# Performance work log

Hardware: AMD Instinct MI355X
Metric: run time of the kernel (lower is better)

## Reference

```python
import jax, jax.numpy as jnp
import numpy as np

N, T, C, G, E = 50000, 2, 768, 16, 800000
H = C // 4          # 192
OUT = 3
EPS = 1e-5


def _lin_init(k, fan_in, fan_out):
    s = 1.0 / np.sqrt(fan_in)
    kw, kb = jax.random.split(k)
    W = jax.random.uniform(kw, (fan_in, fan_out), minval=-s, maxval=s, dtype=jnp.float32)
    b = jax.random.uniform(kb, (fan_out,), minval=-s, maxval=s, dtype=jnp.float32)
    return W, b


def setup_inputs() -> dict:
    key = jax.random.key(0)
    ks = jax.random.split(key, 8)
    x = jax.random.normal(ks[0], (N, T, C), dtype=jnp.float32)
    batch = jnp.sort(jax.random.randint(ks[1], (N,), 0, G))
    edge_index = jax.random.randint(ks[2], (2, E), 0, N)
    W0, b0 = _lin_init(ks[3], C, H)
    W1, b1 = _lin_init(ks[4], H, H)
    Wh1, bh1 = _lin_init(ks[5], H, H)
    Wh2, bh2 = _lin_init(ks[6], H, OUT)
    ones = jnp.ones((H,), jnp.float32)
    zeros = jnp.zeros((H,), jnp.float32)
    return {
        "x": x, "batch": batch, "edge_index": edge_index,
        "W0": W0, "b0": b0, "gn0_w": ones, "gn0_b": zeros, "gn0_a": ones,
        "W1": W1, "b1": b1, "gn1_w": ones, "gn1_b": zeros, "gn1_a": ones,
        "Wh1": Wh1, "bh1": bh1, "Wh2": Wh2, "bh2": bh2,
    }


def _gelu(v):
    return jax.nn.gelu(v, approximate=False)  # torch nn.GELU default = exact erf


def _gcn_conv(h, W, b, src, dst, dinv):
    # PyG GCNConv: x' = D^-1/2 (A+I) D^-1/2 (x W) + b, self-loops added implicitly
    h = jnp.einsum('ntc,cd->ntd', h, W)                       # [N,T,Cout]
    norm = (dinv[src] * dinv[dst])[:, None, None]             # [E,1,1]
    agg = jax.ops.segment_sum(h[src] * norm, dst, num_segments=N)
    agg = agg + h * (dinv * dinv)[:, None, None]              # self-loop term
    return agg + b


def _graph_norm(h, batch, cnt, w, b, alpha):
    # PyG GraphNorm: per-graph mean/var with learnable mean scale
    mean = jax.ops.segment_sum(h, batch, num_segments=G) / cnt   # [G,T,C]
    out = h - alpha * mean[batch]
    var = jax.ops.segment_sum(out * out, batch, num_segments=G) / cnt
    std = jnp.sqrt(var + EPS)
    return w * out / std[batch] + b


def reference(x, batch, edge_index,
              W0, b0, gn0_w, gn0_b, gn0_a,
              W1, b1, gn1_w, gn1_b, gn1_a,
              Wh1, bh1, Wh2, bh2):
    src, dst = edge_index[0], edge_index[1]
    deg = jax.ops.segment_sum(jnp.ones((E,), jnp.float32), dst, num_segments=N) + 1.0
    dinv = jax.lax.rsqrt(deg)
    cnt = jax.ops.segment_sum(jnp.ones((N,), jnp.float32), batch, num_segments=G)[:, None, None]

    # layer 0: 768 -> 192 (no residual, shape mismatch)
    h = _gcn_conv(x, W0, b0, src, dst, dinv)
    h = _gelu(_graph_norm(h, batch, cnt, gn0_w, gn0_b, gn0_a))
    # layer 1: 192 -> 192 with residual
    h_in = h
    h = _gcn_conv(h, W1, b1, src, dst, dinv)
    h = _gelu(_graph_norm(h, batch, cnt, gn1_w, gn1_b, gn1_a))
    h = h + h_in
    # MLP head
    h = _gelu(jnp.einsum('ntc,cd->ntd', h, Wh1) + bh1)
    out = jnp.einsum('ntc,cd->ntd', h, Wh2) + bh2            # [N,T,3]
    return out
```

## Files before the change

### kernel.cpp

```cpp
#include <hip/hip_runtime.h>
#include <math.h>

#define NN   50000
#define TT   2
#define CC   768
#define GG   16
#define EE   800000
#define HH   192
#define OUTD 3
#define MR   (NN*TT)
#define FD   (TT*HH)
#define EPS_GN 1e-5f
#define GN_CHUNK 128
#define AGG_CH 128

typedef __attribute__((ext_vector_type(8))) short bf16x8;
typedef __attribute__((ext_vector_type(4))) float f32x4;

__device__ __forceinline__ float gelu_exact(float x){
    return 0.5f * x * (1.0f + erff(x * 0.70710678118654752440f));
}

__device__ __forceinline__ short f2b(float f){
    unsigned u = __float_as_uint(f);
    unsigned r = (u + 0x7FFFu + ((u>>16)&1u)) >> 16;
    return (short)r;
}
__device__ __forceinline__ float b2f(unsigned short u){
    return __uint_as_float(((unsigned)u)<<16);
}

__global__ __launch_bounds__(256) void k_deg(const int* __restrict__ dst, float* __restrict__ deg){
    int e = blockIdx.x*256 + threadIdx.x;
    if(e < EE) atomicAdd(&deg[dst[e]], 1.0f);
}

__global__ __launch_bounds__(64) void k_cnt2(const int* __restrict__ batch, float* __restrict__ cnt){
    int g = threadIdx.x;
    if(g >= GG) return;
    int lo0=0, hi=NN;
    while(lo0<hi){ int mid=(lo0+hi)>>1; if(batch[mid] < g) lo0=mid+1; else hi=mid; }
    int lo1=lo0; hi=NN;
    while(lo1<hi){ int mid=(lo1+hi)>>1; if(batch[mid] < g+1) lo1=mid+1; else hi=mid; }
    cnt[g] = (float)(lo1 - lo0);
}

__global__ __launch_bounds__(256) void k_dinv(const float* __restrict__ deg, float* __restrict__ dinv){
    int i = blockIdx.x*256 + threadIdx.x;
    if(i < NN) dinv[i] = rsqrtf(deg[i] + 1.0f);
}

__global__ __launch_bounds__(256) void k_wconv(const float* __restrict__ W0, const float* __restrict__ W1,
                                               const float* __restrict__ Wh1,
                                               short* __restrict__ Wt0, short* __restrict__ Wt1,
                                               short* __restrict__ Wth1){
    int i = blockIdx.x*256 + threadIdx.x;
    if(i < CC*HH){
        int k = i / HH, n = i % HH;
        Wt0[(size_t)n*CC + k] = f2b(W0[i]);
    }
    if(i < HH*HH){
        int k = i / HH, n = i % HH;
        Wt1 [(size_t)n*HH + k] = f2b(W1[i]);
        Wth1[(size_t)n*HH + k] = f2b(Wh1[i]);
    }
}

__global__ __launch_bounds__(256) void k_scan1(const float* __restrict__ deg, int* __restrict__ partial){
    __shared__ int s[256];
    int t = threadIdx.x;
    int i = blockIdx.x*256 + t;
    int v = (i < NN) ? (int)deg[i] : 0;
    s[t] = v; __syncthreads();
    for(int off=128; off>0; off>>=1){ if(t < off) s[t] += s[t+off]; __syncthreads(); }
    if(t == 0) partial[blockIdx.x] = s[0];
}

__global__ __launch_bounds__(256) void k_scan2(int* __restrict__ partial){
    __shared__ int s[256];
    int t = threadIdx.x;
    int v = partial[t];
    s[t] = v; __syncthreads();
    for(int off=1; off<256; off<<=1){
        int x = (t >= off) ? s[t-off] : 0;
        __syncthreads();
        s[t] += x;
        __syncthreads();
    }
    partial[t] = s[t] - v;
}

__global__ __launch_bounds__(256) void k_scan3(const float* __restrict__ deg, const int* __restrict__ partial,
                                               int* __restrict__ csr_off){
    __shared__ int s[256];
    int t = threadIdx.x;
    int i = blockIdx.x*256 + t;
    int v = (i < NN) ? (int)deg[i] : 0;
    s[t] = v; __syncthreads();
    for(int off=1; off<256; off<<=1){
        int x = (t >= off) ? s[t-off] : 0;
        __syncthreads();
        s[t] += x;
        __syncthreads();
    }
    if(i < NN) csr_off[i] = partial[blockIdx.x] + s[t] - v;
}

__global__ __launch_bounds__(256) void k_fill(const int* __restrict__ src, const int* __restrict__ dst,
                                              const int* __restrict__ csr_off, int* __restrict__ fillcnt,
                                              int* __restrict__ csr_src){
    int e = blockIdx.x*256 + threadIdx.x;
    if(e < EE){
        int d = dst[e];
        int pos = csr_off[d] + atomicAdd(&fillcnt[d], 1);
        csr_src[pos] = src[e];
    }
}

__device__ __forceinline__ void gn8(const float* __restrict__ src,
                                    const float* __restrict__ sm, const float* __restrict__ sq,
                                    int sb, int hb_,
                                    const float* __restrict__ wg, const float* __restrict__ bg,
                                    const float* __restrict__ ag, float ic, float v[8]){
    float4 u0 = *(const float4*)(src),     u1 = *(const float4*)(src+4);
    float4 m0 = *(const float4*)(sm+sb),   m1 = *(const float4*)(sm+sb+4);
    float4 q0 = *(const float4*)(sq+sb),   q1 = *(const float4*)(sq+sb+4);
    float4 w0 = *(const float4*)(wg+hb_),  w1 = *(const float4*)(wg+hb_+4);
    float4 b0 = *(const float4*)(bg+hb_),  b1 = *(const float4*)(bg+hb_+4);
    float4 a0 = *(const float4*)(ag+hb_),  a1 = *(const float4*)(ag+hb_+4);
    float uu[8]={u0.x,u0.y,u0.z,u0.w,u1.x,u1.y,u1.z,u1.w};
    float mm[8]={m0.x,m0.y,m0.z,m0.w,m1.x,m1.y,m1.z,m1.w};
    float qq[8]={q0.x,q0.y,q0.z,q0.w,q1.x,q1.y,q1.z,q1.w};
    float ww[8]={w0.x,w0.y,w0.z,w0.w,w1.x,w1.y,w1.z,w1.w};
    float bb[8]={b0.x,b0.y,b0.z,b0.w,b1.x,b1.y,b1.z,b1.w};
    float aa[8]={a0.x,a0.y,a0.z,a0.w,a1.x,a1.y,a1.z,a1.w};
    #pragma unroll
    for(int j=0;j<8;j++){
        float mean = mm[j]*ic, ex2 = qq[j]*ic, al = aa[j];
        float var = ex2 - (2.0f*al - al*al)*mean*mean;
        float t = ww[j]*(uu[j] - al*mean)*rsqrtf(var + EPS_GN) + bb[j];
        v[j] = gelu_exact(t);
    }
}

template<int MODE, int NORM, bool BIAS>
__global__ __launch_bounds__(256) void k_gemm_mfma(
        const float* __restrict__ A1, const float* __restrict__ A0,
        const short* __restrict__ Bt,
        const float* __restrict__ bias, void* __restrict__ Cv,
        const float* __restrict__ W2, const float* __restrict__ b2,
        const int* __restrict__ batch, const float* __restrict__ cnt,
        const float* __restrict__ sm1, const float* __restrict__ sq1,
        const float* __restrict__ wg1, const float* __restrict__ bg1, const float* __restrict__ ag1,
        const float* __restrict__ sm0, const float* __restrict__ sq0,
        const float* __restrict__ wg0, const float* __restrict__ bg0, const float* __restrict__ ag0,
        int Mrows, int Kdim){
    __shared__ short As[64][40];
    __shared__ short Bs[192][40];
    int tid = threadIdx.x;
    int bm = blockIdx.x*64;
    int wv = tid>>6, lane = tid&63;
    int lm = lane&15, lq = lane>>4;

    f32x4 acc[12];
    #pragma unroll
    for(int i=0;i<12;i++) acc[i] = (f32x4){0.f,0.f,0.f,0.f};

    int ar = tid>>2, akg = (tid&3)<<3;
    int row = bm + ar;
    bool aok = row < Mrows;
    const float* Ap1 = A1 + (size_t)row*Kdim + akg;
    const float* Ap0 = (NORM==2) ? (A0 + (size_t)row*Kdim + akg) : nullptr;
    int g = 0, tT = 0; float ic = 0.f;
    if(NORM >= 1 && aok){
        int nn = row>>1; tT = row&1;
        g = batch[nn];
        ic = 1.0f / cnt[g];
    }

    for(int k0 = 0; k0 < Kdim; k0 += 32){
        bf16x8 ap = {};
        if(aok){
            if(NORM == 0){
                float4 av0 = *(const float4*)(Ap1 + k0);
                float4 av1 = *(const float4*)(Ap1 + k0 + 4);
                ap[0]=f2b(av0.x); ap[1]=f2b(av0.y); ap[2]=f2b(av0.z); ap[3]=f2b(av0.w);
                ap[4]=f2b(av1.x); ap[5]=f2b(av1.y); ap[6]=f2b(av1.z); ap[7]=f2b(av1.w);
            } else {
                int hb_ = akg + k0;
                int sb  = g*FD + tT*HH + hb_;
                float v[8];
                gn8(Ap1 + k0, sm1, sq1, sb, hb_, wg1, bg1, ag1, ic, v);
                if(NORM == 2){
                    float v0[8];
                    gn8(Ap0 + k0, sm0, sq0, sb, hb_, wg0, bg0, ag0, ic, v0);
                    #pragma unroll
                    for(int j=0;j<8;j++) v[j] += v0[j];
                }
                #pragma unroll
                for(int j=0;j<8;j++) ap[j] = f2b(v[j]);
            }
        }
        bf16x8 bvals[3];
        #pragma unroll
        for(int i=0;i<3;i++){
            int idx = tid + i*256;
            int n = idx>>2, kg = (idx&3)<<3;
            bvals[i] = *(const bf16x8*)(Bt + (size_t)n*Kdim + k0 + kg);
        }
        __syncthreads();
        *(bf16x8*)&As[ar][akg] = ap;
        #pragma unroll
        for(int i=0;i<3;i++){
            int idx = tid + i*256;
            int n = idx>>2, kg = (idx&3)<<3;
            *(bf16x8*)&Bs[n][kg] = bvals[i];
        }
        __syncthreads();
        bf16x8 af = *(const bf16x8*)&As[wv*16 + lm][lq*8];
        #pragma unroll
        for(int ct=0; ct<12; ct++){
            bf16x8 bfr = *(const bf16x8*)&Bs[ct*16 + lm][lq*8];
            acc[ct] = __builtin_amdgcn_mfma_f32_16x16x32_bf16(af, bfr, acc[ct], 0, 0, 0);
        }
    }

    if(MODE == 1){
        short* C = (short*)Cv;
        #pragma unroll
        for(int ct=0; ct<12; ct++){
            int col = ct*16 + lm;
            float bs = BIAS ? bias[col] : 0.f;
            #pragma unroll
            for(int r=0; r<4; r++){
                int orow = bm + wv*16 + lq*4 + r;
                if(orow < Mrows) C[(size_t)orow*HH + col] = f2b(acc[ct][r] + bs);
            }
        }
    } else {
        float hs[4][3] = {};
        #pragma unroll
        for(int ct=0; ct<12; ct++){
            int col = ct*16 + lm;
            float bs = bias[col];
            float w20 = W2[col*3+0], w21 = W2[col*3+1], w22 = W2[col*3+2];
            #pragma unroll
            for(int r=0; r<4; r++){
                float gl = gelu_exact(acc[ct][r] + bs);
                hs[r][0] += gl*w20; hs[r][1] += gl*w21; hs[r][2] += gl*w22;
            }
        }
        #pragma unroll
        for(int off=1; off<16; off<<=1){
            #pragma unroll
            for(int r=0;r<4;r++){
                hs[r][0] += __shfl_xor(hs[r][0], off);
                hs[r][1] += __shfl_xor(hs[r][1], off);
                hs[r][2] += __shfl_xor(hs[r][2], off);
            }
        }
        if(lm == 0){
            float* O = (float*)Cv;
            #pragma unroll
            for(int r=0;r<4;r++){
                int orow = bm + wv*16 + lq*4 + r;
                if(orow < Mrows){
                    O[(size_t)orow*3+0] = hs[r][0] + b2[0];
                    O[(size_t)orow*3+1] = hs[r][1] + b2[1];
                    O[(size_t)orow*3+2] = hs[r][2] + b2[2];
                }
            }
        }
    }
}

__global__ __launch_bounds__(192) void k_agg(const ushort* __restrict__ hw, const int* __restrict__ csr_src,
                                             const int* __restrict__ csr_off, const float* __restrict__ deg,
                                             const float* __restrict__ dinv, const float* __restrict__ bias,
                                             float* __restrict__ out){
    __shared__ int   sidx[AGG_CH];
    __shared__ float swt [AGG_CH];
    int n = blockIdx.x;
    int t = threadIdx.x;
    float di = dinv[n];
    const ushort2* H2 = (const ushort2*)hw;
    ushort2 sv = H2[(size_t)n*192 + t];
    float self = di*di;
    float ax = b2f(sv.x)*self, ay = b2f(sv.y)*self;
    int beg = csr_off[n];
    int end = beg + (int)deg[n];
    for(int base = beg; base < end; base += AGG_CH){
        int m = min(AGG_CH, end - base);
        __syncthreads();
        for(int j = t; j < m; j += 192){
            int s = csr_src[base + j];
            sidx[j] = s;
            swt[j] = dinv[s]*di;
        }
        __syncthreads();
        int j = 0;
        for(; j+4 <= m; j += 4){
            int s0=sidx[j], s1=sidx[j+1], s2=sidx[j+2], s3=sidx[j+3];
            float w0=swt[j], w1=swt[j+1], w2=swt[j+2], w3=swt[j+3];
            ushort2 v0 = H2[(size_t)s0*192 + t];
            ushort2 v1 = H2[(size_t)s1*192 + t];
            ushort2 v2 = H2[(size_t)s2*192 + t];
            ushort2 v3 = H2[(size_t)s3*192 + t];
            ax += w0*b2f(v0.x) + w1*b2f(v1.x) + w2*b2f(v2.x) + w3*b2f(v3.x);
            ay += w0*b2f(v0.y) + w1*b2f(v1.y) + w2*b2f(v2.y) + w3*b2f(v3.y);
        }
        for(; j < m; j++){
            int s = sidx[j]; float ww = swt[j];
            ushort2 v = H2[(size_t)s*192 + t];
            ax += ww*b2f(v.x); ay += ww*b2f(v.y);
        }
    }
    int f = 2*t;
    int hh = (f < HH) ? f : f - HH;
    out[(size_t)n*FD + f]   = ax + bias[hh];
    out[(size_t)n*FD + f+1] = ay + bias[hh+1];
}

__global__ __launch_bounds__(384) void k_gn_stats(const float* __restrict__ h, const int* __restrict__ batch,
                                                  float* __restrict__ ssum, float* __restrict__ ssq){
    int f = threadIdx.x;
    int n0 = blockIdx.x*GN_CHUNK;
    int n1 = min(n0 + GN_CHUNK, NN);
    int g = batch[n0];
    float a = 0.f, a2 = 0.f;
    for(int n = n0; n < n1; n++){
        int gn = batch[n];
        if(gn != g){
            atomicAdd(&ssum[g*FD + f], a);
            atomicAdd(&ssq [g*FD + f], a2);
            a = 0.f; a2 = 0.f; g = gn;
        }
        float v = h[(size_t)n*FD + f];
        a += v; a2 += v*v;
    }
    atomicAdd(&ssum[g*FD + f], a);
    atomicAdd(&ssq [g*FD + f], a2);
}

extern "C" void kernel_launch(void* const* d_in, const int* in_sizes, int n_in,
                              void* d_out, int out_size, void* d_ws, size_t ws_size,
                              hipStream_t stream){
    const float* x     = (const float*)d_in[0];
    const int*   batch = (const int*)d_in[1];
    const int*   ei    = (const int*)d_in[2];
    const int*   src   = ei;
    const int*   dst   = ei + EE;
    const float* W0    = (const float*)d_in[3];
    const float* b0    = (const float*)d_in[4];
    const float* gn0_w = (const float*)d_in[5];
    const float* gn0_b = (const float*)d_in[6];
    const float* gn0_a = (const float*)d_in[7];
    const float* W1    = (const float*)d_in[8];
    const float* b1    = (const float*)d_in[9];
    const float* gn1_w = (const float*)d_in[10];
    const float* gn1_b = (const float*)d_in[11];
    const float* gn1_a = (const float*)d_in[12];
    const float* Wh1   = (const float*)d_in[13];
    const float* bh1   = (const float*)d_in[14];
    const float* Wh2   = (const float*)d_in[15];
    const float* bh2   = (const float*)d_in[16];
    float* out = (float*)d_out;

    char* w = (char*)d_ws;
    auto alloc = [&](size_t bytes)->void*{
        void* p = (void*)w;
        w += (bytes + 255) & ~(size_t)255;
        return p;
    };
    char* zbase = w;
    float* deg     = (float*)alloc((size_t)NN*4);
    int*   fillcnt = (int*)  alloc((size_t)NN*4);
    int*   partial = (int*)  alloc(256*4);
    float* s0m     = (float*)alloc((size_t)GG*FD*4);
    float* s0q     = (float*)alloc((size_t)GG*FD*4);
    float* s1m     = (float*)alloc((size_t)GG*FD*4);
    float* s1q     = (float*)alloc((size_t)GG*FD*4);
    size_t zbytes = (size_t)(w - zbase);
    float* cnt     = (float*)alloc((size_t)GG*4);
    float* dinv    = (float*)alloc((size_t)NN*4);
    int*   csr_off = (int*)  alloc((size_t)NN*4);
    int*   csr_src = (int*)  alloc((size_t)EE*4);
    short* Wt0     = (short*)alloc((size_t)HH*CC*2);
    short* Wt1     = (short*)alloc((size_t)HH*HH*2);
    short* Wth1    = (short*)alloc((size_t)HH*HH*2);
    short* hb0     = (short*)alloc((size_t)MR*HH*2);
    short* hb1     = (short*)alloc((size_t)MR*HH*2);
    float* agg0    = (float*)alloc((size_t)MR*HH*4);
    float* agg1    = (float*)alloc((size_t)MR*HH*4);

    hipMemsetAsync(zbase, 0, zbytes, stream);

    k_deg  <<<(EE+255)/256, 256, 0, stream>>>(dst, deg);
    k_cnt2 <<<1, 64, 0, stream>>>(batch, cnt);
    k_dinv <<<(NN+255)/256, 256, 0, stream>>>(deg, dinv);
    k_wconv<<<(CC*HH+255)/256, 256, 0, stream>>>(W0, W1, Wh1, Wt0, Wt1, Wth1);

    int nscan = (NN+255)/256;
    k_scan1<<<nscan, 256, 0, stream>>>(deg, partial);
    k_scan2<<<1,     256, 0, stream>>>(partial);
    k_scan3<<<nscan, 256, 0, stream>>>(deg, partial, csr_off);
    k_fill <<<(EE+255)/256, 256, 0, stream>>>(src, dst, csr_off, fillcnt, csr_src);

    int gemm_grid = (MR+63)/64;
    int ngn = (NN + GN_CHUNK - 1)/GN_CHUNK;

    k_gemm_mfma<1,0,false><<<gemm_grid, 256, 0, stream>>>(
        x, nullptr, Wt0, nullptr, hb0, nullptr, nullptr,
        nullptr, nullptr,
        nullptr, nullptr, nullptr, nullptr, nullptr,
        nullptr, nullptr, nullptr, nullptr, nullptr, MR, CC);
    k_agg<<<NN, 192, 0, stream>>>((const ushort*)hb0, csr_src, csr_off, deg, dinv, b0, agg0);
    k_gn_stats<<<ngn, 384, 0, stream>>>(agg0, batch, s0m, s0q);

    k_gemm_mfma<1,1,false><<<gemm_grid, 256, 0, stream>>>(
        agg0, nullptr, Wt1, nullptr, hb1, nullptr, nullptr,
        batch, cnt,
        s0m, s0q, gn0_w, gn0_b, gn0_a,
        nullptr, nullptr, nullptr, nullptr, nullptr, MR, HH);
    k_agg<<<NN, 192, 0, stream>>>((const ushort*)hb1, csr_src, csr_off, deg, dinv, b1, agg1);
    k_gn_stats<<<ngn, 384, 0, stream>>>(agg1, batch, s1m, s1q);

    k_gemm_mfma<2,2,true><<<gemm_grid, 256, 0, stream>>>(
        agg1, agg0, Wth1, bh1, out, Wh2, bh2,
        batch, cnt,
        s1m, s1q, gn1_w, gn1_b, gn1_a,
        s0m, s0q, gn0_w, gn0_b, gn0_a, MR, HH);
}
```

Measured before the change: 1.032 ms.

## Prefetch GEMM tiles, unroll gather and stats loops, fuse dinv into scan

Result: faster. 985.9 us (-4.5%).

```diff
diff --git a/kernel.cpp b/kernel.cpp
--- a/kernel.cpp
+++ b/kernel.cpp
@@ -11,7 +11,7 @@
 #define MR   (NN*TT)
 #define FD   (TT*HH)
 #define EPS_GN 1e-5f
-#define GN_CHUNK 128
+#define GN_CHUNK 32
 #define AGG_CH 128
 
 typedef __attribute__((ext_vector_type(8))) short bf16x8;
@@ -45,11 +45,6 @@
     cnt[g] = (float)(lo1 - lo0);
 }
 
-__global__ __launch_bounds__(256) void k_dinv(const float* __restrict__ deg, float* __restrict__ dinv){
-    int i = blockIdx.x*256 + threadIdx.x;
-    if(i < NN) dinv[i] = rsqrtf(deg[i] + 1.0f);
-}
-
 __global__ __launch_bounds__(256) void k_wconv(const float* __restrict__ W0, const float* __restrict__ W1,
                                                const float* __restrict__ Wh1,
                                                short* __restrict__ Wt0, short* __restrict__ Wt1,
@@ -66,11 +61,14 @@
     }
 }
 
-__global__ __launch_bounds__(256) void k_scan1(const float* __restrict__ deg, int* __restrict__ partial){
+__global__ __launch_bounds__(256) void k_scan1(const float* __restrict__ deg, int* __restrict__ partial,
+                                               float* __restrict__ dinv){
     __shared__ int s[256];
     int t = threadIdx.x;
     int i = blockIdx.x*256 + t;
-    int v = (i < NN) ? (int)deg[i] : 0;
+    float dv = (i < NN) ? deg[i] : 0.f;
+    if(i < NN) dinv[i] = rsqrtf(dv + 1.0f);
+    int v = (int)dv;
     s[t] = v; __syncthreads();
     for(int off=128; off>0; off>>=1){ if(t < off) s[t] += s[t+off]; __syncthreads(); }
     if(t == 0) partial[blockIdx.x] = s[0];
@@ -117,12 +115,11 @@
     }
 }
 
-__device__ __forceinline__ void gn8(const float* __restrict__ src,
-                                    const float* __restrict__ sm, const float* __restrict__ sq,
-                                    int sb, int hb_,
-                                    const float* __restrict__ wg, const float* __restrict__ bg,
-                                    const float* __restrict__ ag, float ic, float v[8]){
-    float4 u0 = *(const float4*)(src),     u1 = *(const float4*)(src+4);
+__device__ __forceinline__ void gn8r(float4 u0, float4 u1,
+                                     const float* __restrict__ sm, const float* __restrict__ sq,
+                                     int sb, int hb_,
+                                     const float* __restrict__ wg, const float* __restrict__ bg,
+                                     const float* __restrict__ ag, float ic, float v[8]){
     float4 m0 = *(const float4*)(sm+sb),   m1 = *(const float4*)(sm+sb+4);
     float4 q0 = *(const float4*)(sq+sb),   q1 = *(const float4*)(sq+sb+4);
     float4 w0 = *(const float4*)(wg+hb_),  w1 = *(const float4*)(wg+hb_+4);
@@ -178,22 +175,33 @@
         ic = 1.0f / cnt[g];
     }
 
+    float4 ra0 = make_float4(0,0,0,0), ra1 = ra0, rb0 = ra0, rb1 = ra0;
+    bf16x8 bv[3];
+    if(aok){
+        ra0 = *(const float4*)(Ap1); ra1 = *(const float4*)(Ap1 + 4);
+        if(NORM==2){ rb0 = *(const float4*)(Ap0); rb1 = *(const float4*)(Ap0 + 4); }
+    }
+    #pragma unroll
+    for(int i=0;i<3;i++){
+        int idx = tid + i*256;
+        int n = idx>>2, kg = (idx&3)<<3;
+        bv[i] = *(const bf16x8*)(Bt + (size_t)n*Kdim + kg);
+    }
+
     for(int k0 = 0; k0 < Kdim; k0 += 32){
         bf16x8 ap = {};
         if(aok){
             if(NORM == 0){
-                float4 av0 = *(const float4*)(Ap1 + k0);
-                float4 av1 = *(const float4*)(Ap1 + k0 + 4);
-                ap[0]=f2b(av0.x); ap[1]=f2b(av0.y); ap[2]=f2b(av0.z); ap[3]=f2b(av0.w);
-                ap[4]=f2b(av1.x); ap[5]=f2b(av1.y); ap[6]=f2b(av1.z); ap[7]=f2b(av1.w);
+                ap[0]=f2b(ra0.x); ap[1]=f2b(ra0.y); ap[2]=f2b(ra0.z); ap[3]=f2b(ra0.w);
+                ap[4]=f2b(ra1.x); ap[5]=f2b(ra1.y); ap[6]=f2b(ra1.z); ap[7]=f2b(ra1.w);
             } else {
                 int hb_ = akg + k0;
                 int sb  = g*FD + tT*HH + hb_;
                 float v[8];
-                gn8(Ap1 + k0, sm1, sq1, sb, hb_, wg1, bg1, ag1, ic, v);
+                gn8r(ra0, ra1, sm1, sq1, sb, hb_, wg1, bg1, ag1, ic, v);
                 if(NORM == 2){
                     float v0[8];
-                    gn8(Ap0 + k0, sm0, sq0, sb, hb_, wg0, bg0, ag0, ic, v0);
+                    gn8r(rb0, rb1, sm0, sq0, sb, hb_, wg0, bg0, ag0, ic, v0);
                     #pragma unroll
                     for(int j=0;j<8;j++) v[j] += v0[j];
                 }
@@ -201,22 +209,29 @@
                 for(int j=0;j<8;j++) ap[j] = f2b(v[j]);
             }
         }
-        bf16x8 bvals[3];
-        #pragma unroll
-        for(int i=0;i<3;i++){
-            int idx = tid + i*256;
-            int n = idx>>2, kg = (idx&3)<<3;
-            bvals[i] = *(const bf16x8*)(Bt + (size_t)n*Kdim + k0 + kg);
-        }
+        bf16x8 bw0 = bv[0], bw1 = bv[1], bw2 = bv[2];
         __syncthreads();
         *(bf16x8*)&As[ar][akg] = ap;
-        #pragma unroll
-        for(int i=0;i<3;i++){
-            int idx = tid + i*256;
-            int n = idx>>2, kg = (idx&3)<<3;
-            *(bf16x8*)&Bs[n][kg] = bvals[i];
-        }
-        __syncthreads();
+        {
+            int idx0 = tid, idx1 = tid+256, idx2 = tid+512;
+            *(bf16x8*)&Bs[idx0>>2][(idx0&3)<<3] = bw0;
+            *(bf16x8*)&Bs[idx1>>2][(idx1&3)<<3] = bw1;
+            *(bf16x8*)&Bs[idx2>>2][(idx2&3)<<3] = bw2;
+        }
+        __syncthreads();
+        int k1 = k0 + 32;
+        if(k1 < Kdim){
+            if(aok){
+                ra0 = *(const float4*)(Ap1 + k1); ra1 = *(const float4*)(Ap1 + k1 + 4);
+                if(NORM==2){ rb0 = *(const float4*)(Ap0 + k1); rb1 = *(const float4*)(Ap0 + k1 + 4); }
+            }
+            #pragma unroll
+            for(int i=0;i<3;i++){
+                int idx = tid + i*256;
+                int n = idx>>2, kg = (idx&3)<<3;
+                bv[i] = *(const bf16x8*)(Bt + (size_t)n*Kdim + k1 + kg);
+            }
+        }
         bf16x8 af = *(const bf16x8*)&As[wv*16 + lm][lq*8];
         #pragma unroll
         for(int ct=0; ct<12; ct++){
@@ -299,15 +314,14 @@
         }
         __syncthreads();
         int j = 0;
-        for(; j+4 <= m; j += 4){
-            int s0=sidx[j], s1=sidx[j+1], s2=sidx[j+2], s3=sidx[j+3];
-            float w0=swt[j], w1=swt[j+1], w2=swt[j+2], w3=swt[j+3];
-            ushort2 v0 = H2[(size_t)s0*192 + t];
-            ushort2 v1 = H2[(size_t)s1*192 + t];
-            ushort2 v2 = H2[(size_t)s2*192 + t];
-            ushort2 v3 = H2[(size_t)s3*192 + t];
-            ax += w0*b2f(v0.x) + w1*b2f(v1.x) + w2*b2f(v2.x) + w3*b2f(v3.x);
-            ay += w0*b2f(v0.y) + w1*b2f(v1.y) + w2*b2f(v2.y) + w3*b2f(v3.y);
+        for(; j+8 <= m; j += 8){
+            int   si[8]; float wt[8]; ushort2 vv[8];
+            #pragma unroll
+            for(int q=0;q<8;q++){ si[q]=sidx[j+q]; wt[q]=swt[j+q]; }
+            #pragma unroll
+            for(int q=0;q<8;q++) vv[q] = H2[(size_t)si[q]*192 + t];
+            #pragma unroll
+            for(int q=0;q<8;q++){ ax += wt[q]*b2f(vv[q].x); ay += wt[q]*b2f(vv[q].y); }
         }
         for(; j < m; j++){
             int s = sidx[j]; float ww = swt[j];
@@ -328,7 +342,31 @@
     int n1 = min(n0 + GN_CHUNK, NN);
     int g = batch[n0];
     float a = 0.f, a2 = 0.f;
-    for(int n = n0; n < n1; n++){
+    int n = n0;
+    for(; n+4 <= n1; n += 4){
+        float v0 = h[(size_t)n*FD + f];
+        float v1 = h[(size_t)(n+1)*FD + f];
+        float v2 = h[(size_t)(n+2)*FD + f];
+        float v3 = h[(size_t)(n+3)*FD + f];
+        int b3 = batch[n+3];
+        if(b3 == g){
+            a  += v0+v1+v2+v3;
+            a2 += v0*v0+v1*v1+v2*v2+v3*v3;
+        } else {
+            float vv[4] = {v0,v1,v2,v3};
+            #pragma unroll
+            for(int q=0;q<4;q++){
+                int gn = batch[n+q];
+                if(gn != g){
+                    atomicAdd(&ssum[g*FD + f], a);
+                    atomicAdd(&ssq [g*FD + f], a2);
+                    a = 0.f; a2 = 0.f; g = gn;
+                }
+                a += vv[q]; a2 += vv[q]*vv[q];
+            }
+        }
+    }
+    for(; n < n1; n++){
         int gn = batch[n];
         if(gn != g){
             atomicAdd(&ssum[g*FD + f], a);
@@ -397,11 +435,10 @@
 
     k_deg  <<<(EE+255)/256, 256, 0, stream>>>(dst, deg);
     k_cnt2 <<<1, 64, 0, stream>>>(batch, cnt);
-    k_dinv <<<(NN+255)/256, 256, 0, stream>>>(deg, dinv);
     k_wconv<<<(CC*HH+255)/256, 256, 0, stream>>>(W0, W1, Wh1, Wt0, Wt1, Wth1);
 
     int nscan = (NN+255)/256;
-    k_scan1<<<nscan, 256, 0, stream>>>(deg, partial);
+    k_scan1<<<nscan, 256, 0, stream>>>(deg, partial, dinv);
     k_scan2<<<1,     256, 0, stream>>>(partial);
     k_scan3<<<nscan, 256, 0, stream>>>(deg, partial, csr_off);
     k_fill <<<(EE+255)/256, 256, 0, stream>>>(src, dst, csr_off, fillcnt, csr_src);
```
